# Performance work log

Measured on AMD Instinct MI355X. Metric: run time of the kernel, lower is better.

The kernel has to match this reference:

```python
import jax, jax.numpy as jnp
import numpy as np

N_WIRES = 10
N_BLOCKS = 4
BATCH = 8192
FEAT = 4 * N_WIRES
DIM = 2 ** N_WIRES
BN_EPS = 1e-5

# sign of PauliZ on wire i for each basis state index (wire 0 = most significant bit,
# matching torchquantum's [bsz, 2, 2, ..., 2] state layout)
_k = np.arange(DIM)
_bits = (_k[None, :] >> (N_WIRES - 1 - np.arange(N_WIRES))[:, None]) & 1
SIGNS = jnp.asarray(1.0 - 2.0 * _bits, dtype=jnp.float32)  # [n_wires, 2^n]

H_GATE = jnp.array([[1, 1], [1, -1]], dtype=jnp.complex64) * jnp.complex64(0.70710678)
SX_GATE = jnp.complex64(0.5) * jnp.array([[1 + 1j, 1 - 1j], [1 - 1j, 1 + 1j]], dtype=jnp.complex64)


def rx_mat(theta):
    t = jnp.asarray(theta) * 0.5
    c = jnp.cos(t).astype(jnp.complex64)
    s = (-1j) * jnp.sin(t).astype(jnp.complex64)
    return jnp.stack([jnp.stack([c, s], -1), jnp.stack([s, c], -1)], -2)


def ry_mat(theta):
    t = jnp.asarray(theta) * 0.5
    c = jnp.cos(t).astype(jnp.complex64)
    s = jnp.sin(t).astype(jnp.complex64)
    return jnp.stack([jnp.stack([c, -s], -1), jnp.stack([s, c], -1)], -2)


def rz_mat(theta):
    e = jnp.exp(jnp.complex64(-0.5j) * jnp.asarray(theta).astype(jnp.complex64))
    z = jnp.zeros_like(e)
    return jnp.stack([jnp.stack([e, z], -1), jnp.stack([z, jnp.conj(e)], -1)], -2)


def apply_1q(state, gate, wire):
    # state: [B, 2, 2, ..., 2]; gate: [2,2] (shared) or [B,2,2] (per-sample encoder)
    s = jnp.moveaxis(state, wire + 1, -1)
    if gate.ndim == 3:
        s = jnp.einsum('bij,b...j->b...i', gate, s)
    else:
        s = jnp.einsum('ij,b...j->b...i', gate, s)
    return jnp.moveaxis(s, -1, wire + 1)


def apply_cnot(state, c, t):
    s = jnp.moveaxis(state, (c + 1, t + 1), (-2, -1))  # [..., ctrl, tgt]
    s = jnp.stack([s[..., 0, :], s[..., 1, ::-1]], axis=-2)
    return jnp.moveaxis(s, (-2, -1), (c + 1, t + 1))


def measure_all_z(state):
    probs = (state.real ** 2 + state.imag ** 2).reshape(state.shape[0], -1)  # [B, 2^n]
    return probs @ SIGNS.T  # [B, n_wires]


def encode(state, feats):
    # GeneralEncoder: per wire i apply rx, ry, rz, rx with data angles feats[:, 4i..4i+3]
    for i in range(N_WIRES):
        state = apply_1q(state, rx_mat(feats[:, 4 * i]), i)
        state = apply_1q(state, ry_mat(feats[:, 4 * i + 1]), i)
        state = apply_1q(state, rz_mat(feats[:, 4 * i + 2]), i)
        state = apply_1q(state, rx_mat(feats[:, 4 * i + 3]), i)
    return state


def qnn(feats, rz1, ry1, rz2, rz3):
    B = feats.shape[0]
    state = jnp.zeros((B, DIM), jnp.complex64).at[:, 0].set(1.0)
    state = state.reshape((B,) + (2,) * N_WIRES)
    for k in range(N_BLOCKS):
        for i in range(N_WIRES):
            state = apply_1q(state, rz_mat(rz1[k, i]), i)
        for i in range(N_WIRES):
            state = apply_1q(state, ry_mat(ry1[k, i]), i)
        for i in range(N_WIRES):
            state = apply_1q(state, rz_mat(rz2[k, i]), i)
        for i in range(N_WIRES):  # circular CNOT ring
            state = apply_cnot(state, i, (i + 1) % N_WIRES)
        if k != N_BLOCKS - 1:
            state = encode(state, feats)
    outs = [measure_all_z(state)]
    for i in range(N_WIRES):
        state = apply_1q(state, H_GATE, i)
    outs.append(measure_all_z(state))
    for i in range(N_WIRES):
        state = apply_1q(state, H_GATE, i)
        state = apply_1q(state, SX_GATE, i)
    outs.append(measure_all_z(state))
    for i in range(N_WIRES):  # only the last rz3 layer is applied in the source
        state = apply_1q(state, rz_mat(rz3[-1, i]), i)
    outs.append(measure_all_z(state))
    return jnp.concatenate(outs, axis=-1)  # [B, 4*n_wires]


def setup_inputs() -> dict:
    key = jax.random.key(0)
    ks = jax.random.split(key, 13)
    pi = np.float32(np.pi)
    w_scale = 1.0 / np.sqrt(np.float32(FEAT))
    return {
        'x': jax.random.normal(ks[0], (BATCH, FEAT), jnp.float32),
        'qlin_w': jax.random.normal(ks[1], (FEAT, FEAT), jnp.float32) * w_scale,
        'qlin_b': jax.random.normal(ks[2], (FEAT,), jnp.float32) * w_scale,
        'bn_gamma': jnp.ones((FEAT,), jnp.float32),
        'bn_beta': jnp.zeros((FEAT,), jnp.float32),
        'clin_w': jax.random.normal(ks[3], (FEAT, FEAT), jnp.float32) * w_scale,
        'clin_b': jax.random.normal(ks[4], (FEAT,), jnp.float32) * w_scale,
        'lin_w': jax.random.normal(ks[5], (FEAT, 2 * FEAT), jnp.float32) * w_scale,
        'lin_b': jax.random.normal(ks[6], (FEAT,), jnp.float32) * w_scale,
        'rz1': jax.random.uniform(ks[7], (N_BLOCKS, N_WIRES), jnp.float32, -pi, pi),
        'ry1': jax.random.uniform(ks[8], (N_BLOCKS, N_WIRES), jnp.float32, -pi, pi),
        'rz2': jax.random.uniform(ks[9], (N_BLOCKS, N_WIRES), jnp.float32, -pi, pi),
        'rz3': jax.random.uniform(ks[10], (N_BLOCKS, N_WIRES), jnp.float32, -pi, pi),
    }


def reference(x, qlin_w, qlin_b, bn_gamma, bn_beta, clin_w, clin_b, lin_w, lin_b, rz1, ry1, rz2, rz3):
    # quantum branch: Linear -> BatchNorm1d (training-mode batch stats) -> QNN
    xq = x @ qlin_w.T + qlin_b
    mu = xq.mean(axis=0)
    var = ((xq - mu) ** 2).mean(axis=0)  # biased variance, as torch BN
    xq = (xq - mu) * jax.lax.rsqrt(var + BN_EPS) * bn_gamma + bn_beta
    x1 = qnn(xq, rz1, ry1, rz2, rz3)
    # classical branch
    x2 = jax.nn.relu(x @ clin_w.T + clin_b)
    return jnp.concatenate([x1, x2], axis=-1) @ lin_w.T + lin_b
```

## Files before the change

### kernel.cpp

```cpp
#include <hip/hip_runtime.h>
#include <math.h>


typedef float v2f __attribute__((ext_vector_type(2)));

#define WS_XQ    0
#define WS_X1    327680
#define WS_PS1   327680
#define WS_PS2   368640
#define WS_BNA   655360
#define WS_BNC   655400
#define WS_GATES 655440

__device__ __forceinline__ float bperm1(int addr, float v){
  return __int_as_float(__builtin_amdgcn_ds_bpermute(addr, __float_as_int(v)));
}
__device__ __forceinline__ v2f bperm2(int addr, v2f v){
  v2f r; r.x = bperm1(addr, v.x); r.y = bperm1(addr, v.y); return r;
}
__device__ __forceinline__ v2f vs(float x){ return (v2f){x,x}; }


__device__ __forceinline__ void g_cross(v2f (&R)[8], v2f (&I)[8],
                                        int addr, bool hi, const float* g)
{
  const float gar = hi ? g[6] : g[0], gai = hi ? g[7] : g[1];
  const float gbr = hi ? g[4] : g[2], gbi = hi ? g[5] : g[3];
  const v2f A=vs(gar), B=vs(gai), C=vs(gbr), D=vs(gbi);
#pragma unroll
  for (int p=0;p<8;++p) {
    v2f PR = bperm2(addr, R[p]);
    v2f PI = bperm2(addr, I[p]);
    v2f nr = A*R[p] - B*I[p] + C*PR - D*PI;
    v2f ni = A*I[p] + B*R[p] + C*PI + D*PR;
    R[p]=nr; I[p]=ni;
  }
}

template<int PM>
__device__ __forceinline__ void g_localp(v2f (&R)[8], v2f (&I)[8], const float* g)
{
  const v2f g00r=vs(g[0]), g00i=vs(g[1]), g01r=vs(g[2]), g01i=vs(g[3]);
  const v2f g10r=vs(g[4]), g10i=vs(g[5]), g11r=vs(g[6]), g11i=vs(g[7]);
#pragma unroll
  for (int p=0;p<8;++p) if (!(p&PM)) {
    const int q = p|PM;
    v2f r0=R[p], i0=I[p], r1=R[q], i1=I[q];
    R[p] = g00r*r0 - g00i*i0 + g01r*r1 - g01i*i1;
    I[p] = g00r*i0 + g00i*r0 + g01r*i1 + g01i*r1;
    R[q] = g10r*r0 - g10i*i0 + g11r*r1 - g11i*i1;
    I[q] = g10r*i0 + g10i*r0 + g11r*i1 + g11i*r1;
  }
}

__device__ __forceinline__ void g_local9(v2f (&R)[8], v2f (&I)[8], const float* g)
{
  const v2f Gr0 = (v2f){g[0], g[4]};
  const v2f Gi0 = (v2f){g[1], g[5]};
  const v2f Gr1 = (v2f){g[2], g[6]};
  const v2f Gi1 = (v2f){g[3], g[7]};
#pragma unroll
  for (int p=0;p<8;++p) {
    v2f Rx = vs(R[p].x), Ix = vs(I[p].x);
    v2f Ry = vs(R[p].y), Iy = vs(I[p].y);
    R[p] = Gr0*Rx - Gi0*Ix + Gr1*Ry - Gi1*Iy;
    I[p] = Gr0*Ix + Gi0*Rx + Gr1*Iy + Gi1*Ry;
  }
}

__device__ __forceinline__ void cnot_ring(v2f (&R)[8], v2f (&I)[8],
                                          int addrg, int a0, bool c5)
{
#pragma unroll
  for (int p=0;p<8;++p) R[p] = bperm2(addrg, R[p]);
#pragma unroll
  for (int p=0;p<8;++p) I[p] = bperm2(addrg, I[p]);
#pragma unroll
  for (int p=0;p<4;++p) {
    v2f a=R[p], b=R[p|4];
    R[p]   = c5 ? b : a;
    R[p|4] = c5 ? a : b;
    v2f ai=I[p], bi=I[p|4];
    I[p]   = c5 ? bi : ai;
    I[p|4] = c5 ? ai : bi;
  }
#pragma unroll
  for (int p=0;p<8;++p) if ((p&4)&&!(p&2)) {
    const int q=p|2;
    v2f t=R[p]; R[p]=R[q]; R[q]=t;
    t=I[p]; I[p]=I[q]; I[q]=t;
  }
#pragma unroll
  for (int p=0;p<8;++p) if ((p&2)&&!(p&1)) {
    const int q=p|1;
    v2f t=R[p]; R[p]=R[q]; R[q]=t;
    t=I[p]; I[p]=I[q]; I[q]=t;
  }
#pragma unroll
  for (int p=1;p<8;p+=2) {
    R[p] = __builtin_shufflevector(R[p],R[p],1,0);
    I[p] = __builtin_shufflevector(I[p],I[p],1,0);
  }
#pragma unroll
  for (int p=0;p<8;++p) {
    R[p].y = bperm1(a0, R[p].y);
    I[p].y = bperm1(a0, I[p].y);
  }
}


__device__ __forceinline__ float wsum(float x, int a0,int a1,int a2,int a3,int a4,int a5)
{
  x += bperm1(a5,x); x += bperm1(a4,x); x += bperm1(a3,x);
  x += bperm1(a2,x); x += bperm1(a1,x); x += bperm1(a0,x);
  return x;
}


__global__ __launch_bounds__(320) void k_xq(const float* __restrict__ x,
                     const float* __restrict__ w, const float* __restrict__ b,
                     float* __restrict__ xq, float* __restrict__ ps1, float* __restrict__ ps2)
{
  __shared__ float wlds[40*41];
  __shared__ float xlds[320];
  __shared__ float accs[320];
  const int t = threadIdx.x;
  const int sl = t/40, f = t - sl*40;
  const int s0 = blockIdx.x*8;
#pragma unroll
  for (int i=0;i<5;++i) {
    int idx = t + i*320;
    int ff = idx/40, kk = idx - ff*40;
    wlds[ff*41+kk] = w[idx];
  }
  xlds[t] = x[s0*40 + t];
  __syncthreads();
  float acc = b[f];
#pragma unroll
  for (int k=0;k<40;++k) acc = fmaf(xlds[sl*40+k], wlds[f*41+k], acc);
  xq[s0*40 + t] = acc;
  accs[t] = acc;
  __syncthreads();
  if (t < 40) {
    float s1=0.f, s2=0.f;
#pragma unroll
    for (int m=0;m<8;++m){ float vv=accs[m*40+t]; s1+=vv; s2=fmaf(vv,vv,s2); }
    ps1[t*1024 + blockIdx.x] = s1;
    ps2[t*1024 + blockIdx.x] = s2;
  }
}

__global__ void k_bn(const float* __restrict__ ps1, const float* __restrict__ ps2,
                     const float* __restrict__ gamma, const float* __restrict__ beta,
                     const float* __restrict__ rz1, const float* __restrict__ ry1,
                     const float* __restrict__ rz2,
                     float* __restrict__ bn_a, float* __restrict__ bn_c,
                     float* __restrict__ gates)
{
  const int f = blockIdx.x, t = threadIdx.x;
  if (f == 40) {
    if (t < 40) {
      float g = rz1[t], a = ry1[t], b = rz2[t];
      float ca, sa, cp, sp, cm, sm;
      sincosf(0.5f*a, &sa, &ca);
      sincosf(0.5f*(b+g), &sp, &cp);
      sincosf(0.5f*(b-g), &sm, &cm);
      float* G = gates + t*8;
      G[0]= ca*cp; G[1]=-ca*sp;
      G[2]=-sa*cm; G[3]= sa*sm;
      G[4]= sa*cm; G[5]= sa*sm;
      G[6]= ca*cp; G[7]= ca*sp;
    }
    return;
  }
  float s1=0.f, s2=0.f;
#pragma unroll
  for (int i=0;i<4;++i){ s1 += ps1[f*1024 + t + i*256]; s2 += ps2[f*1024 + t + i*256]; }
  __shared__ float a1[256], a2[256];
  a1[t]=s1; a2[t]=s2; __syncthreads();
  for (int off=128; off; off>>=1){
    if (t<off){ a1[t]+=a1[t+off]; a2[t]+=a2[t+off]; }
    __syncthreads();
  }
  if (t==0) {
    float mu = a1[0]*(1.f/8192.f);
    float var = a2[0]*(1.f/8192.f) - mu*mu;
    float a = gamma[f]*rsqrtf(var + 1e-5f);
    bn_a[f]=a; bn_c[f]=beta[f]-mu*a;
  }
}

#define GEN10(PTR) \
  g_cross(R,I,a0,h0,(PTR)+0);  g_cross(R,I,a1,h1,(PTR)+8);  \
  g_cross(R,I,a2,h2,(PTR)+16); g_cross(R,I,a3,h3,(PTR)+24); \
  g_cross(R,I,a4,h4,(PTR)+32); g_cross(R,I,a5,h5,(PTR)+40); \
  g_localp<4>(R,I,(PTR)+48);   g_localp<2>(R,I,(PTR)+56);   \
  g_localp<1>(R,I,(PTR)+64);   g_local9(R,I,(PTR)+72);

__global__ __launch_bounds__(256) void k_qnn(const float* __restrict__ xq,
    const float* __restrict__ bn_a, const float* __restrict__ bn_c,
    const float* __restrict__ gates, float* __restrict__ x1)
{
  const int lane = threadIdx.x & 63;
  const int wv   = threadIdx.x >> 6;
  const int s    = blockIdx.x*4 + wv;

  __shared__ float Ebuf[4][10][8];
  __shared__ float Fbuf[4][3][10][8];

  if (lane < 10) {
    const int i = lane;
    const int f = 4*i;
    float h0 = 0.5f * fmaf(xq[s*40+f+0], bn_a[f+0], bn_c[f+0]);
    float h1 = 0.5f * fmaf(xq[s*40+f+1], bn_a[f+1], bn_c[f+1]);
    float h2 = 0.5f * fmaf(xq[s*40+f+2], bn_a[f+2], bn_c[f+2]);
    float h3 = 0.5f * fmaf(xq[s*40+f+3], bn_a[f+3], bn_c[f+3]);
    float c0,s0,c1,s1,c2,s2,c3,s3;
    sincosf(h0,&s0,&c0); sincosf(h1,&s1,&c1);
    sincosf(h2,&s2,&c2); sincosf(h3,&s3,&c3);
    float A00r=c1*c0, A00i= s1*s0;
    float A01r=-s1*c0, A01i=-c1*s0;
    float A10r= s1*c0, A10i=-c1*s0;
    float A11r= c1*c0, A11i=-s1*s0;
    float B00r = A00r*c2 + A00i*s2, B00i = A00i*c2 - A00r*s2;
    float B01r = A01r*c2 + A01i*s2, B01i = A01i*c2 - A01r*s2;
    float B10r = A10r*c2 - A10i*s2, B10i = A10i*c2 + A10r*s2;
    float B11r = A11r*c2 - A11i*s2, B11i = A11i*c2 + A11r*s2;
    float* e = &Ebuf[wv][i][0];
    e[0] = c3*B00r + s3*B10i;  e[1] = c3*B00i - s3*B10r;
    e[2] = c3*B01r + s3*B11i;  e[3] = c3*B01i - s3*B11r;
    e[4] = c3*B10r + s3*B00i;  e[5] = c3*B10i - s3*B00r;
    e[6] = c3*B11r + s3*B01i;  e[7] = c3*B11i - s3*B01r;
  }
  __syncthreads();

  if (lane < 30) {
    const int k = lane/10, i = lane - k*10;
    const float* U = gates + (k+1)*80 + i*8;
    const float* E = &Ebuf[wv][i][0];
    float u00r=U[0],u00i=U[1],u01r=U[2],u01i=U[3],u10r=U[4],u10i=U[5],u11r=U[6],u11i=U[7];
    float e00r=E[0],e00i=E[1],e01r=E[2],e01i=E[3],e10r=E[4],e10i=E[5],e11r=E[6],e11i=E[7];
    float* F = &Fbuf[wv][k][i][0];
    F[0] = u00r*e00r - u00i*e00i + u01r*e10r - u01i*e10i;
    F[1] = u00r*e00i + u00i*e00r + u01r*e10i + u01i*e10r;
    F[2] = u00r*e01r - u00i*e01i + u01r*e11r - u01i*e11i;
    F[3] = u00r*e01i + u00i*e01r + u01r*e11i + u01i*e11r;
    F[4] = u10r*e00r - u10i*e00i + u11r*e10r - u11i*e10i;
    F[5] = u10r*e00i + u10i*e00r + u11r*e10i + u11i*e10r;
    F[6] = u10r*e01r - u10i*e01i + u11r*e11r - u11i*e11i;
    F[7] = u10r*e01i + u10i*e01r + u11r*e11i + u11i*e11r;
  }
  __syncthreads();

  const int a0 = ((lane ^ 32) << 2);
  const int a1 = ((lane ^ 16) << 2);
  const int a2 = ((lane ^  8) << 2);
  const int a3 = ((lane ^  4) << 2);
  const int a4 = ((lane ^  2) << 2);
  const int a5 = ((lane ^  1) << 2);
  const bool h0 = (lane & 32) != 0;
  const bool h1 = (lane & 16) != 0;
  const bool h2 = (lane &  8) != 0;
  const bool h3 = (lane &  4) != 0;
  const bool h4 = (lane &  2) != 0;
  const bool h5 = (lane &  1) != 0;
  const int addrg = (lane ^ (lane >> 1)) << 2;

  v2f R[8], I[8];
  {
    float cr = 1.f, ci = 0.f;
#pragma unroll
    for (int w=0; w<6; ++w) {
      const float g0r = gates[w*8+0], g0i = gates[w*8+1];
      const float g1r = gates[w*8+4], g1i = gates[w*8+5];
      const bool bset = (lane >> (5-w)) & 1;
      const float ar = bset ? g1r : g0r, ai = bset ? g1i : g0i;
      const float tr = cr*ar - ci*ai, ti = cr*ai + ci*ar;
      cr = tr; ci = ti;
    }
    float p67r[4], p67i[4], p89r[4], p89i[4];
#pragma unroll
    for (int b6=0;b6<2;++b6)
#pragma unroll
      for (int b7=0;b7<2;++b7) {
        const float x6r = gates[6*8 + 4*b6], x6i = gates[6*8 + 4*b6 + 1];
        const float x7r = gates[7*8 + 4*b7], x7i = gates[7*8 + 4*b7 + 1];
        p67r[b6*2+b7] = x6r*x7r - x6i*x7i;
        p67i[b6*2+b7] = x6r*x7i + x6i*x7r;
      }
#pragma unroll
    for (int b8=0;b8<2;++b8)
#pragma unroll
      for (int b9=0;b9<2;++b9) {
        const float x8r = gates[8*8 + 4*b8], x8i = gates[8*8 + 4*b8 + 1];
        const float x9r = gates[9*8 + 4*b9], x9i = gates[9*8 + 4*b9 + 1];
        p89r[b8*2+b9] = x8r*x9r - x8i*x9i;
        p89i[b8*2+b9] = x8r*x9i + x8i*x9r;
      }
#pragma unroll
    for (int m=0;m<4;++m) {
      const float tr = p67r[m]*cr - p67i[m]*ci;
      const float ti = p67r[m]*ci + p67i[m]*cr;
      p67r[m]=tr; p67i[m]=ti;
    }
#pragma unroll
    for (int p=0;p<8;++p) {
      const int hi = p>>1, b8 = p&1;
      const v2f Pr = (v2f){p89r[2*b8], p89r[2*b8+1]};
      const v2f Pi = (v2f){p89i[2*b8], p89i[2*b8+1]};
      R[p] = vs(p67r[hi])*Pr - vs(p67i[hi])*Pi;
      I[p] = vs(p67r[hi])*Pi + vs(p67i[hi])*Pr;
    }
  }

  cnot_ring(R,I,addrg,a0,h5);
  { const float* F = &Fbuf[wv][0][0][0]; GEN10(F) }
  cnot_ring(R,I,addrg,a0,h5);
  { const float* F = &Fbuf[wv][1][0][0]; GEN10(F) }
  cnot_ring(R,I,addrg,a0,h5);
  { const float* F = &Fbuf[wv][2][0][0]; GEN10(F) }
  cnot_ring(R,I,addrg,a0,h5);

  float* dst = x1 + s*40;

  {
    v2f pv[8];
#pragma unroll
    for (int p=0;p<8;++p) pv[p] = R[p]*R[p] + I[p]*I[p];
    v2f T8 = (pv[0]-pv[1]) + (pv[2]-pv[3]) + (pv[4]-pv[5]) + (pv[6]-pv[7]);
    v2f aa[4];
#pragma unroll
    for (int m=0;m<4;++m) aa[m] = pv[2*m] + pv[2*m+1];
    v2f T7 = (aa[0]-aa[1]) + (aa[2]-aa[3]);
    v2f T6 = (aa[0]+aa[1]) - (aa[2]+aa[3]);
    v2f S  = (aa[0]+aa[1]) + (aa[2]+aa[3]);
    float q8 = T8.x + T8.y;
    float q7 = T7.x + T7.y;
    float q6 = T6.x + T6.y;
    float q9 = S.x - S.y;
    float P  = S.x + S.y;

    float v = P;
    { float pt = bperm1(a5,v); v = (lane& 1) ? (pt - v) : (pt + v); }
    { float pt = bperm1(a4,v); v = (lane& 2) ? (pt - v) : (pt + v); }
    { float pt = bperm1(a3,v); v = (lane& 4) ? (pt - v) : (pt + v); }
    { float pt = bperm1(a2,v); v = (lane& 8) ? (pt - v) : (pt + v); }
    { float pt = bperm1(a1,v); v = (lane&16) ? (pt - v) : (pt + v); }
    { float pt = bperm1(a0,v); v = (lane&32) ? (pt - v) : (pt + v); }

    q6 = wsum(q6,a0,a1,a2,a3,a4,a5);
    q7 = wsum(q7,a0,a1,a2,a3,a4,a5);
    q8 = wsum(q8,a0,a1,a2,a3,a4,a5);
    q9 = wsum(q9,a0,a1,a2,a3,a4,a5);

    if (lane==32) dst[0]=v;
    if (lane==16) dst[1]=v;
    if (lane== 8) dst[2]=v;
    if (lane== 4) dst[3]=v;
    if (lane== 2) dst[4]=v;
    if (lane== 1) dst[5]=v;
    if (lane== 0){ dst[6]=q6; dst[7]=q7; dst[8]=q8; dst[9]=q9; }
  }

#define XYC(AW,HW,W) { \
    v2f U=vs(0.f), V=vs(0.f); \
    _Pragma("unroll") \
    for (int p=0;p<8;++p) { \
      v2f PR = bperm2(AW, R[p]); \
      v2f PI = bperm2(AW, I[p]); \
      U += R[p]*PR + I[p]*PI; \
      V += I[p]*PR - R[p]*PI; \
    } \
    float u = U.x + U.y; \
    float vv = V.x + V.y; \
    vv = (HW) ? vv : -vv; \
    u  = wsum(u ,a0,a1,a2,a3,a4,a5); \
    vv = wsum(vv,a0,a1,a2,a3,a4,a5); \
    if (lane==0){ dst[10+(W)]=u; dst[20+(W)]=vv; dst[30+(W)]=vv; } \
  }
  XYC(a0,h0,0) XYC(a1,h1,1) XYC(a2,h2,2)
  XYC(a3,h3,3) XYC(a4,h4,4) XYC(a5,h5,5)
#undef XYC

#define XYL(PM,W) { \
    v2f U=vs(0.f), V=vs(0.f); \
    _Pragma("unroll") \
    for (int p=0;p<8;++p) if (!(p&(PM))) { \
      const int q=p|(PM); \
      U += R[p]*R[q] + I[p]*I[q]; \
      V += I[p]*R[q] - R[p]*I[q]; \
    } \
    float u = U.x + U.y; \
    float vv = V.x + V.y; \
    u  = wsum(u ,a0,a1,a2,a3,a4,a5); \
    vv = wsum(vv,a0,a1,a2,a3,a4,a5); \
    if (lane==0){ dst[10+(W)]=2.f*u; float y=-2.f*vv; dst[20+(W)]=y; dst[30+(W)]=y; } \
  }
  XYL(4,6) XYL(2,7) XYL(1,8)
#undef XYL

  {
    float u=0.f, vv=0.f;
#pragma unroll
    for (int p=0;p<8;++p) {
      u  = fmaf(R[p].x, R[p].y, u);  u  = fmaf(I[p].x, I[p].y, u);
      vv = fmaf(I[p].x, R[p].y, vv); vv = fmaf(-R[p].x, I[p].y, vv);
    }
    u  = wsum(u ,a0,a1,a2,a3,a4,a5);
    vv = wsum(vv,a0,a1,a2,a3,a4,a5);
    if (lane==0){ dst[19]=2.f*u; float y=-2.f*vv; dst[29]=y; dst[39]=y; }
  }
}

__global__ void k_epi(const float* __restrict__ x, const float* __restrict__ x1,
                      const float* __restrict__ clin_w, const float* __restrict__ clin_b,
                      const float* __restrict__ lin_w, const float* __restrict__ lin_b,
                      float* __restrict__ out)
{
  const int t = threadIdx.x;
  const int sl = t/40, f = t - sl*40;
  const int s = blockIdx.x*8 + sl;
  __shared__ float x2s[8][40];
  float acc = clin_b[f];
#pragma unroll
  for (int k=0;k<40;++k) acc = fmaf(x[s*40+k], clin_w[f*40+k], acc);
  x2s[sl][f] = fmaxf(acc, 0.f);
  __syncthreads();
  float o = lin_b[f];
#pragma unroll
  for (int j=0;j<40;++j) o = fmaf(x1[s*40+j], lin_w[f*80+j], o);
#pragma unroll
  for (int j=0;j<40;++j) o = fmaf(x2s[sl][j], lin_w[f*80+40+j], o);
  out[s*40+f] = o;
}

extern "C" void kernel_launch(void* const* d_in, const int* in_sizes, int n_in,
                              void* d_out, int out_size, void* d_ws, size_t ws_size,
                              hipStream_t stream)
{
  const float* x      = (const float*)d_in[0];
  const float* qlin_w = (const float*)d_in[1];
  const float* qlin_b = (const float*)d_in[2];
  const float* bn_g   = (const float*)d_in[3];
  const float* bn_b   = (const float*)d_in[4];
  const float* clin_w = (const float*)d_in[5];
  const float* clin_b = (const float*)d_in[6];
  const float* lin_w  = (const float*)d_in[7];
  const float* lin_b  = (const float*)d_in[8];
  const float* rz1    = (const float*)d_in[9];
  const float* ry1    = (const float*)d_in[10];
  const float* rz2    = (const float*)d_in[11];

  float* ws    = (float*)d_ws;
  float* xq    = ws + WS_XQ;
  float* x1    = ws + WS_X1;
  float* ps1   = ws + WS_PS1;
  float* ps2   = ws + WS_PS2;
  float* bn_a  = ws + WS_BNA;
  float* bn_c  = ws + WS_BNC;
  float* gates = ws + WS_GATES;
  float* out   = (float*)d_out;

  hipLaunchKernelGGL(k_xq,  dim3(1024), dim3(320), 0, stream, x, qlin_w, qlin_b, xq, ps1, ps2);
  hipLaunchKernelGGL(k_bn,  dim3(41),   dim3(256), 0, stream, ps1, ps2, bn_g, bn_b,
                     rz1, ry1, rz2, bn_a, bn_c, gates);
  hipLaunchKernelGGL(k_qnn, dim3(2048), dim3(256), 0, stream, xq, bn_a, bn_c, gates, x1);
  hipLaunchKernelGGL(k_epi, dim3(1024), dim3(320), 0, stream, x, x1, clin_w, clin_b, lin_w, lin_b, out);
}
```

Measured before the change: 198.4 us.

## Fold BN stats and gate setup into QNN kernel; use DPP for lane shuffles

The separate BN-reduction/gate kernel is removed. k_xq now adds per-block feature sums into an 80-float accumulator with atomics, zeroed by a memset. Each k_qnn block then computes the BN scale/shift and gate matrices into shared memory itself. In k_qnn, the xor-1 and xor-2 lane exchanges and all wave reductions use DPP quad-perm and row-shift/broadcast ops instead of ds_bpermute, and two intra-wave barriers are dropped. This trades a kernel launch and LDS-routed permutes for redundant per-block setup work, float atomics with nondeterministic summation order, and an extra memset.

```diff
diff --git a/kernel.cpp b/kernel.cpp
--- a/kernel.cpp
+++ b/kernel.cpp
@@ -6,11 +6,7 @@
 
 #define WS_XQ    0
 #define WS_X1    327680
-#define WS_PS1   327680
-#define WS_PS2   368640
-#define WS_BNA   655360
-#define WS_BNC   655400
-#define WS_GATES 655440
+#define WS_BNACC 655360
 
 __device__ __forceinline__ float bperm1(int addr, float v){
   return __int_as_float(__builtin_amdgcn_ds_bpermute(addr, __float_as_int(v)));
@@ -19,6 +15,27 @@
   v2f r; r.x = bperm1(addr, v.x); r.y = bperm1(addr, v.y); return r;
 }
 __device__ __forceinline__ v2f vs(float x){ return (v2f){x,x}; }
+
+template<int C>
+__device__ __forceinline__ float dppf(float x){
+  return __int_as_float(__builtin_amdgcn_update_dpp(0, __float_as_int(x),
+                                                    C, 0xf, 0xf, true));
+}
+template<int C>
+__device__ __forceinline__ v2f dpp2(v2f v){
+  v2f r; r.x = dppf<C>(v.x); r.y = dppf<C>(v.y); return r;
+}
+__device__ __forceinline__ float dsum(float x){
+  x += dppf<0x111>(x);
+  x += dppf<0x112>(x);
+  x += dppf<0x114>(x);
+  x += dppf<0x118>(x);
+  x += dppf<0x142>(x);
+  x += dppf<0x143>(x);
+  return x;
+}
+#define QP_X1 0xB1
+#define QP_X2 0x4E
 
 
 __device__ __forceinline__ void g_cross(v2f (&R)[8], v2f (&I)[8],
@@ -31,6 +48,23 @@
   for (int p=0;p<8;++p) {
     v2f PR = bperm2(addr, R[p]);
     v2f PI = bperm2(addr, I[p]);
+    v2f nr = A*R[p] - B*I[p] + C*PR - D*PI;
+    v2f ni = A*I[p] + B*R[p] + C*PI + D*PR;
+    R[p]=nr; I[p]=ni;
+  }
+}
+
+template<int QP>
+__device__ __forceinline__ void g_cross_dpp(v2f (&R)[8], v2f (&I)[8],
+                                            bool hi, const float* g)
+{
+  const float gar = hi ? g[6] : g[0], gai = hi ? g[7] : g[1];
+  const float gbr = hi ? g[4] : g[2], gbi = hi ? g[5] : g[3];
+  const v2f A=vs(gar), B=vs(gai), C=vs(gbr), D=vs(gbi);
+#pragma unroll
+  for (int p=0;p<8;++p) {
+    v2f PR = dpp2<QP>(R[p]);
+    v2f PI = dpp2<QP>(I[p]);
     v2f nr = A*R[p] - B*I[p] + C*PR - D*PI;
     v2f ni = A*I[p] + B*R[p] + C*PI + D*PR;
     R[p]=nr; I[p]=ni;
@@ -109,17 +143,9 @@
 }
 
 
-__device__ __forceinline__ float wsum(float x, int a0,int a1,int a2,int a3,int a4,int a5)
-{
-  x += bperm1(a5,x); x += bperm1(a4,x); x += bperm1(a3,x);
-  x += bperm1(a2,x); x += bperm1(a1,x); x += bperm1(a0,x);
-  return x;
-}
-
-
 __global__ __launch_bounds__(320) void k_xq(const float* __restrict__ x,
                      const float* __restrict__ w, const float* __restrict__ b,
-                     float* __restrict__ xq, float* __restrict__ ps1, float* __restrict__ ps2)
+                     float* __restrict__ xq, float* __restrict__ bn_acc)
 {
   __shared__ float wlds[40*41];
   __shared__ float xlds[320];
@@ -145,76 +171,62 @@
     float s1=0.f, s2=0.f;
 #pragma unroll
     for (int m=0;m<8;++m){ float vv=accs[m*40+t]; s1+=vv; s2=fmaf(vv,vv,s2); }
-    ps1[t*1024 + blockIdx.x] = s1;
-    ps2[t*1024 + blockIdx.x] = s2;
-  }
-}
-
-__global__ void k_bn(const float* __restrict__ ps1, const float* __restrict__ ps2,
-                     const float* __restrict__ gamma, const float* __restrict__ beta,
-                     const float* __restrict__ rz1, const float* __restrict__ ry1,
-                     const float* __restrict__ rz2,
-                     float* __restrict__ bn_a, float* __restrict__ bn_c,
-                     float* __restrict__ gates)
-{
-  const int f = blockIdx.x, t = threadIdx.x;
-  if (f == 40) {
-    if (t < 40) {
-      float g = rz1[t], a = ry1[t], b = rz2[t];
-      float ca, sa, cp, sp, cm, sm;
-      sincosf(0.5f*a, &sa, &ca);
-      sincosf(0.5f*(b+g), &sp, &cp);
-      sincosf(0.5f*(b-g), &sm, &cm);
-      float* G = gates + t*8;
-      G[0]= ca*cp; G[1]=-ca*sp;
-      G[2]=-sa*cm; G[3]= sa*sm;
-      G[4]= sa*cm; G[5]= sa*sm;
-      G[6]= ca*cp; G[7]= ca*sp;
-    }
-    return;
-  }
-  float s1=0.f, s2=0.f;
-#pragma unroll
-  for (int i=0;i<4;++i){ s1 += ps1[f*1024 + t + i*256]; s2 += ps2[f*1024 + t + i*256]; }
-  __shared__ float a1[256], a2[256];
-  a1[t]=s1; a2[t]=s2; __syncthreads();
-  for (int off=128; off; off>>=1){
-    if (t<off){ a1[t]+=a1[t+off]; a2[t]+=a2[t+off]; }
-    __syncthreads();
-  }
-  if (t==0) {
-    float mu = a1[0]*(1.f/8192.f);
-    float var = a2[0]*(1.f/8192.f) - mu*mu;
-    float a = gamma[f]*rsqrtf(var + 1e-5f);
-    bn_a[f]=a; bn_c[f]=beta[f]-mu*a;
+    atomicAdd(&bn_acc[t],    s1);
+    atomicAdd(&bn_acc[40+t], s2);
   }
 }
 
 #define GEN10(PTR) \
   g_cross(R,I,a0,h0,(PTR)+0);  g_cross(R,I,a1,h1,(PTR)+8);  \
   g_cross(R,I,a2,h2,(PTR)+16); g_cross(R,I,a3,h3,(PTR)+24); \
-  g_cross(R,I,a4,h4,(PTR)+32); g_cross(R,I,a5,h5,(PTR)+40); \
+  g_cross_dpp<QP_X2>(R,I,h4,(PTR)+32); \
+  g_cross_dpp<QP_X1>(R,I,h5,(PTR)+40); \
   g_localp<4>(R,I,(PTR)+48);   g_localp<2>(R,I,(PTR)+56);   \
   g_localp<1>(R,I,(PTR)+64);   g_local9(R,I,(PTR)+72);
 
 __global__ __launch_bounds__(256) void k_qnn(const float* __restrict__ xq,
-    const float* __restrict__ bn_a, const float* __restrict__ bn_c,
-    const float* __restrict__ gates, float* __restrict__ x1)
-{
-  const int lane = threadIdx.x & 63;
-  const int wv   = threadIdx.x >> 6;
+    const float* __restrict__ bn_acc,
+    const float* __restrict__ gamma, const float* __restrict__ beta,
+    const float* __restrict__ rz1, const float* __restrict__ ry1,
+    const float* __restrict__ rz2, float* __restrict__ x1)
+{
+  const int tix  = threadIdx.x;
+  const int lane = tix & 63;
+  const int wv   = tix >> 6;
   const int s    = blockIdx.x*4 + wv;
 
+  __shared__ float Gbuf[40][8];
+  __shared__ float bnA[40], bnC[40];
   __shared__ float Ebuf[4][10][8];
   __shared__ float Fbuf[4][3][10][8];
+
+  if (tix < 40) {
+    float s1 = bn_acc[tix], s2 = bn_acc[40+tix];
+    float mu = s1*(1.f/8192.f);
+    float var = s2*(1.f/8192.f) - mu*mu;
+    float a = gamma[tix]*rsqrtf(var + 1e-5f);
+    bnA[tix]=a; bnC[tix]=beta[tix]-mu*a;
+
+    float g = rz1[tix], ay = ry1[tix], bz = rz2[tix];
+    float ca, sa, cp, sp, cm, sm;
+    sincosf(0.5f*ay, &sa, &ca);
+    sincosf(0.5f*(bz+g), &sp, &cp);
+    sincosf(0.5f*(bz-g), &sm, &cm);
+    float* G = &Gbuf[tix][0];
+    G[0]= ca*cp; G[1]=-ca*sp;
+    G[2]=-sa*cm; G[3]= sa*sm;
+    G[4]= sa*cm; G[5]= sa*sm;
+    G[6]= ca*cp; G[7]= ca*sp;
+  }
+  __syncthreads();
 
   if (lane < 10) {
     const int i = lane;
     const int f = 4*i;
-    float h0 = 0.5f * fmaf(xq[s*40+f+0], bn_a[f+0], bn_c[f+0]);
-    float h1 = 0.5f * fmaf(xq[s*40+f+1], bn_a[f+1], bn_c[f+1]);
-    float h2 = 0.5f * fmaf(xq[s*40+f+2], bn_a[f+2], bn_c[f+2]);
-    float h3 = 0.5f * fmaf(xq[s*40+f+3], bn_a[f+3], bn_c[f+3]);
+    float h0 = 0.5f * fmaf(xq[s*40+f+0], bnA[f+0], bnC[f+0]);
+    float h1 = 0.5f * fmaf(xq[s*40+f+1], bnA[f+1], bnC[f+1]);
+    float h2 = 0.5f * fmaf(xq[s*40+f+2], bnA[f+2], bnC[f+2]);
+    float h3 = 0.5f * fmaf(xq[s*40+f+3], bnA[f+3], bnC[f+3]);
     float c0,s0,c1,s1,c2,s2,c3,s3;
     sincosf(h0,&s0,&c0); sincosf(h1,&s1,&c1);
     sincosf(h2,&s2,&c2); sincosf(h3,&s3,&c3);
@@ -232,11 +244,10 @@
     e[4] = c3*B10r + s3*B00i;  e[5] = c3*B10i - s3*B00r;
     e[6] = c3*B11r + s3*B01i;  e[7] = c3*B11i - s3*B01r;
   }
-  __syncthreads();
 
   if (lane < 30) {
     const int k = lane/10, i = lane - k*10;
-    const float* U = gates + (k+1)*80 + i*8;
+    const float* U = &Gbuf[(k+1)*10 + i][0];
     const float* E = &Ebuf[wv][i][0];
     float u00r=U[0],u00i=U[1],u01r=U[2],u01i=U[3],u10r=U[4],u10i=U[5],u11r=U[6],u11i=U[7];
     float e00r=E[0],e00i=E[1],e01r=E[2],e01i=E[3],e10r=E[4],e10i=E[5],e11r=E[6],e11i=E[7];
@@ -250,14 +261,11 @@
     F[6] = u10r*e01r - u10i*e01i + u11r*e11r - u11i*e11i;
     F[7] = u10r*e01i + u10i*e01r + u11r*e11i + u11i*e11r;
   }
-  __syncthreads();
 
   const int a0 = ((lane ^ 32) << 2);
   const int a1 = ((lane ^ 16) << 2);
   const int a2 = ((lane ^  8) << 2);
   const int a3 = ((lane ^  4) << 2);
-  const int a4 = ((lane ^  2) << 2);
-  const int a5 = ((lane ^  1) << 2);
   const bool h0 = (lane & 32) != 0;
   const bool h1 = (lane & 16) != 0;
   const bool h2 = (lane &  8) != 0;
@@ -271,8 +279,8 @@
     float cr = 1.f, ci = 0.f;
 #pragma unroll
     for (int w=0; w<6; ++w) {
-      const float g0r = gates[w*8+0], g0i = gates[w*8+1];
-      const float g1r = gates[w*8+4], g1i = gates[w*8+5];
+      const float g0r = Gbuf[w][0], g0i = Gbuf[w][1];
+      const float g1r = Gbuf[w][4], g1i = Gbuf[w][5];
       const bool bset = (lane >> (5-w)) & 1;
       const float ar = bset ? g1r : g0r, ai = bset ? g1i : g0i;
       const float tr = cr*ar - ci*ai, ti = cr*ai + ci*ar;
@@ -283,8 +291,8 @@
     for (int b6=0;b6<2;++b6)
 #pragma unroll
       for (int b7=0;b7<2;++b7) {
-        const float x6r = gates[6*8 + 4*b6], x6i = gates[6*8 + 4*b6 + 1];
-        const float x7r = gates[7*8 + 4*b7], x7i = gates[7*8 + 4*b7 + 1];
+        const float x6r = Gbuf[6][4*b6], x6i = Gbuf[6][4*b6+1];
+        const float x7r = Gbuf[7][4*b7], x7i = Gbuf[7][4*b7+1];
         p67r[b6*2+b7] = x6r*x7r - x6i*x7i;
         p67i[b6*2+b7] = x6r*x7i + x6i*x7r;
       }
@@ -292,8 +300,8 @@
     for (int b8=0;b8<2;++b8)
 #pragma unroll
       for (int b9=0;b9<2;++b9) {
-        const float x8r = gates[8*8 + 4*b8], x8i = gates[8*8 + 4*b8 + 1];
-        const float x9r = gates[9*8 + 4*b9], x9i = gates[9*8 + 4*b9 + 1];
+        const float x8r = Gbuf[8][4*b8], x8i = Gbuf[8][4*b8+1];
+        const float x9r = Gbuf[9][4*b9], x9i = Gbuf[9][4*b9+1];
         p89r[b8*2+b9] = x8r*x9r - x8i*x9i;
         p89i[b8*2+b9] = x8r*x9i + x8i*x9r;
       }
@@ -341,17 +349,14 @@
     float P  = S.x + S.y;
 
     float v = P;
-    { float pt = bperm1(a5,v); v = (lane& 1) ? (pt - v) : (pt + v); }
-    { float pt = bperm1(a4,v); v = (lane& 2) ? (pt - v) : (pt + v); }
-    { float pt = bperm1(a3,v); v = (lane& 4) ? (pt - v) : (pt + v); }
-    { float pt = bperm1(a2,v); v = (lane& 8) ? (pt - v) : (pt + v); }
-    { float pt = bperm1(a1,v); v = (lane&16) ? (pt - v) : (pt + v); }
-    { float pt = bperm1(a0,v); v = (lane&32) ? (pt - v) : (pt + v); }
-
-    q6 = wsum(q6,a0,a1,a2,a3,a4,a5);
-    q7 = wsum(q7,a0,a1,a2,a3,a4,a5);
-    q8 = wsum(q8,a0,a1,a2,a3,a4,a5);
-    q9 = wsum(q9,a0,a1,a2,a3,a4,a5);
+    { float pt = dppf<QP_X1>(v); v = (lane& 1) ? (pt - v) : (pt + v); }
+    { float pt = dppf<QP_X2>(v); v = (lane& 2) ? (pt - v) : (pt + v); }
+    { float pt = bperm1(a3,v);   v = (lane& 4) ? (pt - v) : (pt + v); }
+    { float pt = bperm1(a2,v);   v = (lane& 8) ? (pt - v) : (pt + v); }
+    { float pt = bperm1(a1,v);   v = (lane&16) ? (pt - v) : (pt + v); }
+    { float pt = bperm1(a0,v);   v = (lane&32) ? (pt - v) : (pt + v); }
+
+    q6 = dsum(q6); q7 = dsum(q7); q8 = dsum(q8); q9 = dsum(q9);
 
     if (lane==32) dst[0]=v;
     if (lane==16) dst[1]=v;
@@ -359,7 +364,7 @@
     if (lane== 4) dst[3]=v;
     if (lane== 2) dst[4]=v;
     if (lane== 1) dst[5]=v;
-    if (lane== 0){ dst[6]=q6; dst[7]=q7; dst[8]=q8; dst[9]=q9; }
+    if (lane==63){ dst[6]=q6; dst[7]=q7; dst[8]=q8; dst[9]=q9; }
   }
 
 #define XYC(AW,HW,W) { \
@@ -374,13 +379,28 @@
     float u = U.x + U.y; \
     float vv = V.x + V.y; \
     vv = (HW) ? vv : -vv; \
-    u  = wsum(u ,a0,a1,a2,a3,a4,a5); \
-    vv = wsum(vv,a0,a1,a2,a3,a4,a5); \
-    if (lane==0){ dst[10+(W)]=u; dst[20+(W)]=vv; dst[30+(W)]=vv; } \
-  }
-  XYC(a0,h0,0) XYC(a1,h1,1) XYC(a2,h2,2)
-  XYC(a3,h3,3) XYC(a4,h4,4) XYC(a5,h5,5)
+    u = dsum(u); vv = dsum(vv); \
+    if (lane==63){ dst[10+(W)]=u; dst[20+(W)]=vv; dst[30+(W)]=vv; } \
+  }
+  XYC(a0,h0,0) XYC(a1,h1,1) XYC(a2,h2,2) XYC(a3,h3,3)
 #undef XYC
+#define XYD(QP,HW,W) { \
+    v2f U=vs(0.f), V=vs(0.f); \
+    _Pragma("unroll") \
+    for (int p=0;p<8;++p) { \
+      v2f PR = dpp2<QP>(R[p]); \
+      v2f PI = dpp2<QP>(I[p]); \
+      U += R[p]*PR + I[p]*PI; \
+      V += I[p]*PR - R[p]*PI; \
+    } \
+    float u = U.x + U.y; \
+    float vv = V.x + V.y; \
+    vv = (HW) ? vv : -vv; \
+    u = dsum(u); vv = dsum(vv); \
+    if (lane==63){ dst[10+(W)]=u; dst[20+(W)]=vv; dst[30+(W)]=vv; } \
+  }
+  XYD(QP_X2,h4,4) XYD(QP_X1,h5,5)
+#undef XYD
 
 #define XYL(PM,W) { \
     v2f U=vs(0.f), V=vs(0.f); \
@@ -392,9 +412,8 @@
     } \
     float u = U.x + U.y; \
     float vv = V.x + V.y; \
-    u  = wsum(u ,a0,a1,a2,a3,a4,a5); \
-    vv = wsum(vv,a0,a1,a2,a3,a4,a5); \
-    if (lane==0){ dst[10+(W)]=2.f*u; float y=-2.f*vv; dst[20+(W)]=y; dst[30+(W)]=y; } \
+    u = dsum(u); vv = dsum(vv); \
+    if (lane==63){ dst[10+(W)]=2.f*u; float y=-2.f*vv; dst[20+(W)]=y; dst[30+(W)]=y; } \
   }
   XYL(4,6) XYL(2,7) XYL(1,8)
 #undef XYL
@@ -406,9 +425,8 @@
       u  = fmaf(R[p].x, R[p].y, u);  u  = fmaf(I[p].x, I[p].y, u);
       vv = fmaf(I[p].x, R[p].y, vv); vv = fmaf(-R[p].x, I[p].y, vv);
     }
-    u  = wsum(u ,a0,a1,a2,a3,a4,a5);
-    vv = wsum(vv,a0,a1,a2,a3,a4,a5);
-    if (lane==0){ dst[19]=2.f*u; float y=-2.f*vv; dst[29]=y; dst[39]=y; }
+    u = dsum(u); vv = dsum(vv);
+    if (lane==63){ dst[19]=2.f*u; float y=-2.f*vv; dst[29]=y; dst[39]=y; }
   }
 }
 
@@ -451,19 +469,15 @@
   const float* ry1    = (const float*)d_in[10];
   const float* rz2    = (const float*)d_in[11];
 
-  float* ws    = (float*)d_ws;
-  float* xq    = ws + WS_XQ;
-  float* x1    = ws + WS_X1;
-  float* ps1   = ws + WS_PS1;
-  float* ps2   = ws + WS_PS2;
-  float* bn_a  = ws + WS_BNA;
-  float* bn_c  = ws + WS_BNC;
-  float* gates = ws + WS_GATES;
-  float* out   = (float*)d_out;
-
-  hipLaunchKernelGGL(k_xq,  dim3(1024), dim3(320), 0, stream, x, qlin_w, qlin_b, xq, ps1, ps2);
-  hipLaunchKernelGGL(k_bn,  dim3(41),   dim3(256), 0, stream, ps1, ps2, bn_g, bn_b,
-                     rz1, ry1, rz2, bn_a, bn_c, gates);
-  hipLaunchKernelGGL(k_qnn, dim3(2048), dim3(256), 0, stream, xq, bn_a, bn_c, gates, x1);
+  float* ws     = (float*)d_ws;
+  float* xq     = ws + WS_XQ;
+  float* x1     = ws + WS_X1;
+  float* bn_acc = ws + WS_BNACC;
+  float* out    = (float*)d_out;
+
+  hipMemsetAsync(bn_acc, 0, 80*sizeof(float), stream);
+  hipLaunchKernelGGL(k_xq,  dim3(1024), dim3(320), 0, stream, x, qlin_w, qlin_b, xq, bn_acc);
+  hipLaunchKernelGGL(k_qnn, dim3(2048), dim3(256), 0, stream, xq, bn_acc, bn_g, bn_b,
+                     rz1, ry1, rz2, x1);
   hipLaunchKernelGGL(k_epi, dim3(1024), dim3(320), 0, stream, x, x1, clin_w, clin_b, lin_w, lin_b, out);
 }
```

Measured after the change: 209.4 us. 1.06x slower.

## Replace ds_bpermute lane exchanges with DPP and permlane swaps in QNN kernel

Applied to the files above, without the earlier changes.

The fixed-distance xor lane exchanges used by the cross-lane gates, the CNOT ring and the expectation reductions now use DPP quad_perm and row_shl/row_shr moves plus permlane16/32 swaps. The old path used ds_bpermute through the LDS pipeline. Wave reductions become a DPP row_shr prefix followed by row_bcast, so the result lands in lane 63 and the stores move to that lane. Two block-level barriers between the per-wave gate-matrix setup stages are removed because each wave only touches its own shared-memory slice. This trades LDS-path latency for VALU work, at the cost of relying on hardware-specific DPP semantics and on implicit in-wave ordering of LDS accesses.

```diff
diff --git a/kernel.cpp b/kernel.cpp
--- a/kernel.cpp
+++ b/kernel.cpp
@@ -3,6 +3,7 @@
 
 
 typedef float v2f __attribute__((ext_vector_type(2)));
+typedef unsigned uiv2 __attribute__((ext_vector_type(2)));
 
 #define WS_XQ    0
 #define WS_X1    327680
@@ -20,22 +21,83 @@
 }
 __device__ __forceinline__ v2f vs(float x){ return (v2f){x,x}; }
 
-
-__device__ __forceinline__ void g_cross(v2f (&R)[8], v2f (&I)[8],
-                                        int addr, bool hi, const float* g)
-{
-  const float gar = hi ? g[6] : g[0], gai = hi ? g[7] : g[1];
-  const float gbr = hi ? g[4] : g[2], gbi = hi ? g[5] : g[3];
-  const v2f A=vs(gar), B=vs(gai), C=vs(gbr), D=vs(gbi);
-#pragma unroll
-  for (int p=0;p<8;++p) {
-    v2f PR = bperm2(addr, R[p]);
-    v2f PI = bperm2(addr, I[p]);
-    v2f nr = A*R[p] - B*I[p] + C*PR - D*PI;
-    v2f ni = A*I[p] + B*R[p] + C*PI + D*PR;
-    R[p]=nr; I[p]=ni;
-  }
-}
+template<int C>
+__device__ __forceinline__ float dppf(float x){
+  return __int_as_float(__builtin_amdgcn_update_dpp(0, __float_as_int(x),
+                                                    C, 0xf, 0xf, true));
+}
+#define QP_X1 0xB1
+#define QP_X2 0x4E
+
+__device__ __forceinline__ float xor1f(float x, int ){ return dppf<QP_X1>(x); }
+__device__ __forceinline__ float xor2f(float x, int ){ return dppf<QP_X2>(x); }
+
+template<int N>
+__device__ __forceinline__ float xorshf(float x, int lane){
+  float a = dppf<0x110+N>(x);
+  float b = dppf<0x100+N>(x);
+  return (lane & N) ? a : b;
+}
+__device__ __forceinline__ float xor4f(float x, int lane){ return xorshf<4>(x,lane); }
+__device__ __forceinline__ float xor8f(float x, int lane){ return xorshf<8>(x,lane); }
+
+#if __has_builtin(__builtin_amdgcn_permlane16_swap) && __has_builtin(__builtin_amdgcn_permlane32_swap)
+__device__ __forceinline__ float xor16f(float x, int lane){
+  uiv2 r = __builtin_amdgcn_permlane16_swap(__float_as_uint(x), __float_as_uint(x),
+                                            false, false);
+  return __uint_as_float((lane & 16) ? r.x : r.y);
+}
+__device__ __forceinline__ float xor32f(float x, int lane){
+  uiv2 r = __builtin_amdgcn_permlane32_swap(__float_as_uint(x), __float_as_uint(x),
+                                            false, false);
+  return __uint_as_float((lane & 32) ? r.x : r.y);
+}
+#else
+__device__ __forceinline__ float xor16f(float x, int lane){ return bperm1((lane^16)<<2, x); }
+__device__ __forceinline__ float xor32f(float x, int lane){ return bperm1((lane^32)<<2, x); }
+#endif
+
+#define DEF_XORV(NAME, F1) \
+__device__ __forceinline__ v2f NAME(v2f v, int lane){ \
+  v2f r; r.x = F1(v.x,lane); r.y = F1(v.y,lane); return r; }
+DEF_XORV(xor1v,  xor1f)
+DEF_XORV(xor2v,  xor2f)
+DEF_XORV(xor4v,  xor4f)
+DEF_XORV(xor8v,  xor8f)
+DEF_XORV(xor16v, xor16f)
+DEF_XORV(xor32v, xor32f)
+
+__device__ __forceinline__ float dsum(float x){
+  x += dppf<0x111>(x);
+  x += dppf<0x112>(x);
+  x += dppf<0x114>(x);
+  x += dppf<0x118>(x);
+  x += dppf<0x142>(x);
+  x += dppf<0x143>(x);
+  return x;
+}
+
+
+#define DEF_GCROSS(NAME, PFN) \
+__device__ __forceinline__ void NAME(v2f (&R)[8], v2f (&I)[8], int lane, bool hi, \
+                                     const float* g){ \
+  const float gar = hi ? g[6] : g[0], gai = hi ? g[7] : g[1]; \
+  const float gbr = hi ? g[4] : g[2], gbi = hi ? g[5] : g[3]; \
+  const v2f A=vs(gar), B=vs(gai), C=vs(gbr), D=vs(gbi); \
+  _Pragma("unroll") \
+  for (int p=0;p<8;++p){ \
+    v2f PR = PFN(R[p],lane); \
+    v2f PI = PFN(I[p],lane); \
+    v2f nr = A*R[p] - B*I[p] + C*PR - D*PI; \
+    v2f ni = A*I[p] + B*R[p] + C*PI + D*PR; \
+    R[p]=nr; I[p]=ni; } \
+}
+DEF_GCROSS(g_cross_x32, xor32v)
+DEF_GCROSS(g_cross_x16, xor16v)
+DEF_GCROSS(g_cross_x8,  xor8v)
+DEF_GCROSS(g_cross_x4,  xor4v)
+DEF_GCROSS(g_cross_x2,  xor2v)
+DEF_GCROSS(g_cross_x1,  xor1v)
 
 template<int PM>
 __device__ __forceinline__ void g_localp(v2f (&R)[8], v2f (&I)[8], const float* g)
@@ -69,7 +131,7 @@
 }
 
 __device__ __forceinline__ void cnot_ring(v2f (&R)[8], v2f (&I)[8],
-                                          int addrg, int a0, bool c5)
+                                          int addrg, int lane, bool c5)
 {
 #pragma unroll
   for (int p=0;p<8;++p) R[p] = bperm2(addrg, R[p]);
@@ -103,17 +165,9 @@
   }
 #pragma unroll
   for (int p=0;p<8;++p) {
-    R[p].y = bperm1(a0, R[p].y);
-    I[p].y = bperm1(a0, I[p].y);
-  }
-}
-
-
-__device__ __forceinline__ float wsum(float x, int a0,int a1,int a2,int a3,int a4,int a5)
-{
-  x += bperm1(a5,x); x += bperm1(a4,x); x += bperm1(a3,x);
-  x += bperm1(a2,x); x += bperm1(a1,x); x += bperm1(a0,x);
-  return x;
+    R[p].y = xor32f(R[p].y, lane);
+    I[p].y = xor32f(I[p].y, lane);
+  }
 }
 
 
@@ -191,9 +245,9 @@
 }
 
 #define GEN10(PTR) \
-  g_cross(R,I,a0,h0,(PTR)+0);  g_cross(R,I,a1,h1,(PTR)+8);  \
-  g_cross(R,I,a2,h2,(PTR)+16); g_cross(R,I,a3,h3,(PTR)+24); \
-  g_cross(R,I,a4,h4,(PTR)+32); g_cross(R,I,a5,h5,(PTR)+40); \
+  g_cross_x32(R,I,lane,h0,(PTR)+0);  g_cross_x16(R,I,lane,h1,(PTR)+8);  \
+  g_cross_x8 (R,I,lane,h2,(PTR)+16); g_cross_x4 (R,I,lane,h3,(PTR)+24); \
+  g_cross_x2 (R,I,lane,h4,(PTR)+32); g_cross_x1 (R,I,lane,h5,(PTR)+40); \
   g_localp<4>(R,I,(PTR)+48);   g_localp<2>(R,I,(PTR)+56);   \
   g_localp<1>(R,I,(PTR)+64);   g_local9(R,I,(PTR)+72);
 
@@ -201,8 +255,9 @@
     const float* __restrict__ bn_a, const float* __restrict__ bn_c,
     const float* __restrict__ gates, float* __restrict__ x1)
 {
-  const int lane = threadIdx.x & 63;
-  const int wv   = threadIdx.x >> 6;
+  const int tix  = threadIdx.x;
+  const int lane = tix & 63;
+  const int wv   = tix >> 6;
   const int s    = blockIdx.x*4 + wv;
 
   __shared__ float Ebuf[4][10][8];
@@ -232,7 +287,6 @@
     e[4] = c3*B10r + s3*B00i;  e[5] = c3*B10i - s3*B00r;
     e[6] = c3*B11r + s3*B01i;  e[7] = c3*B11i - s3*B01r;
   }
-  __syncthreads();
 
   if (lane < 30) {
     const int k = lane/10, i = lane - k*10;
@@ -250,14 +304,7 @@
     F[6] = u10r*e01r - u10i*e01i + u11r*e11r - u11i*e11i;
     F[7] = u10r*e01i + u10i*e01r + u11r*e11i + u11i*e11r;
   }
-  __syncthreads();
-
-  const int a0 = ((lane ^ 32) << 2);
-  const int a1 = ((lane ^ 16) << 2);
-  const int a2 = ((lane ^  8) << 2);
-  const int a3 = ((lane ^  4) << 2);
-  const int a4 = ((lane ^  2) << 2);
-  const int a5 = ((lane ^  1) << 2);
+
   const bool h0 = (lane & 32) != 0;
   const bool h1 = (lane & 16) != 0;
   const bool h2 = (lane &  8) != 0;
@@ -313,13 +360,13 @@
     }
   }
 
-  cnot_ring(R,I,addrg,a0,h5);
+  cnot_ring(R,I,addrg,lane,h5);
   { const float* F = &Fbuf[wv][0][0][0]; GEN10(F) }
-  cnot_ring(R,I,addrg,a0,h5);
+  cnot_ring(R,I,addrg,lane,h5);
   { const float* F = &Fbuf[wv][1][0][0]; GEN10(F) }
-  cnot_ring(R,I,addrg,a0,h5);
+  cnot_ring(R,I,addrg,lane,h5);
   { const float* F = &Fbuf[wv][2][0][0]; GEN10(F) }
-  cnot_ring(R,I,addrg,a0,h5);
+  cnot_ring(R,I,addrg,lane,h5);
 
   float* dst = x1 + s*40;
 
@@ -341,17 +388,14 @@
     float P  = S.x + S.y;
 
     float v = P;
-    { float pt = bperm1(a5,v); v = (lane& 1) ? (pt - v) : (pt + v); }
-    { float pt = bperm1(a4,v); v = (lane& 2) ? (pt - v) : (pt + v); }
-    { float pt = bperm1(a3,v); v = (lane& 4) ? (pt - v) : (pt + v); }
-    { float pt = bperm1(a2,v); v = (lane& 8) ? (pt - v) : (pt + v); }
-    { float pt = bperm1(a1,v); v = (lane&16) ? (pt - v) : (pt + v); }
-    { float pt = bperm1(a0,v); v = (lane&32) ? (pt - v) : (pt + v); }
-
-    q6 = wsum(q6,a0,a1,a2,a3,a4,a5);
-    q7 = wsum(q7,a0,a1,a2,a3,a4,a5);
-    q8 = wsum(q8,a0,a1,a2,a3,a4,a5);
-    q9 = wsum(q9,a0,a1,a2,a3,a4,a5);
+    { float pt = xor1f (v,lane); v = h5 ? (pt - v) : (pt + v); }
+    { float pt = xor2f (v,lane); v = h4 ? (pt - v) : (pt + v); }
+    { float pt = xor4f (v,lane); v = h3 ? (pt - v) : (pt + v); }
+    { float pt = xor8f (v,lane); v = h2 ? (pt - v) : (pt + v); }
+    { float pt = xor16f(v,lane); v = h1 ? (pt - v) : (pt + v); }
+    { float pt = xor32f(v,lane); v = h0 ? (pt - v) : (pt + v); }
+
+    q6 = dsum(q6); q7 = dsum(q7); q8 = dsum(q8); q9 = dsum(q9);
 
     if (lane==32) dst[0]=v;
     if (lane==16) dst[1]=v;
@@ -359,27 +403,26 @@
     if (lane== 4) dst[3]=v;
     if (lane== 2) dst[4]=v;
     if (lane== 1) dst[5]=v;
-    if (lane== 0){ dst[6]=q6; dst[7]=q7; dst[8]=q8; dst[9]=q9; }
-  }
-
-#define XYC(AW,HW,W) { \
+    if (lane==63){ dst[6]=q6; dst[7]=q7; dst[8]=q8; dst[9]=q9; }
+  }
+
+#define XYC(PFN,HW,W) { \
     v2f U=vs(0.f), V=vs(0.f); \
     _Pragma("unroll") \
     for (int p=0;p<8;++p) { \
-      v2f PR = bperm2(AW, R[p]); \
-      v2f PI = bperm2(AW, I[p]); \
+      v2f PR = PFN(R[p],lane); \
+      v2f PI = PFN(I[p],lane); \
       U += R[p]*PR + I[p]*PI; \
       V += I[p]*PR - R[p]*PI; \
     } \
     float u = U.x + U.y; \
     float vv = V.x + V.y; \
     vv = (HW) ? vv : -vv; \
-    u  = wsum(u ,a0,a1,a2,a3,a4,a5); \
-    vv = wsum(vv,a0,a1,a2,a3,a4,a5); \
-    if (lane==0){ dst[10+(W)]=u; dst[20+(W)]=vv; dst[30+(W)]=vv; } \
-  }
-  XYC(a0,h0,0) XYC(a1,h1,1) XYC(a2,h2,2)
-  XYC(a3,h3,3) XYC(a4,h4,4) XYC(a5,h5,5)
+    u = dsum(u); vv = dsum(vv); \
+    if (lane==63){ dst[10+(W)]=u; dst[20+(W)]=vv; dst[30+(W)]=vv; } \
+  }
+  XYC(xor32v,h0,0) XYC(xor16v,h1,1) XYC(xor8v,h2,2)
+  XYC(xor4v ,h3,3) XYC(xor2v ,h4,4) XYC(xor1v,h5,5)
 #undef XYC
 
 #define XYL(PM,W) { \
@@ -392,9 +435,8 @@
     } \
     float u = U.x + U.y; \
     float vv = V.x + V.y; \
-    u  = wsum(u ,a0,a1,a2,a3,a4,a5); \
-    vv = wsum(vv,a0,a1,a2,a3,a4,a5); \
-    if (lane==0){ dst[10+(W)]=2.f*u; float y=-2.f*vv; dst[20+(W)]=y; dst[30+(W)]=y; } \
+    u = dsum(u); vv = dsum(vv); \
+    if (lane==63){ dst[10+(W)]=2.f*u; float y=-2.f*vv; dst[20+(W)]=y; dst[30+(W)]=y; } \
   }
   XYL(4,6) XYL(2,7) XYL(1,8)
 #undef XYL
@@ -406,9 +448,8 @@
       u  = fmaf(R[p].x, R[p].y, u);  u  = fmaf(I[p].x, I[p].y, u);
       vv = fmaf(I[p].x, R[p].y, vv); vv = fmaf(-R[p].x, I[p].y, vv);
     }
-    u  = wsum(u ,a0,a1,a2,a3,a4,a5);
-    vv = wsum(vv,a0,a1,a2,a3,a4,a5);
-    if (lane==0){ dst[19]=2.f*u; float y=-2.f*vv; dst[29]=y; dst[39]=y; }
+    u = dsum(u); vv = dsum(vv);
+    if (lane==63){ dst[19]=2.f*u; float y=-2.f*vv; dst[29]=y; dst[39]=y; }
   }
 }
 
```

Measured after the change: 177.5 us. 10.6% less time.
